# Kernel tuning notes

Measured on AMD Instinct MI355X. Metric: run time of the kernel, lower is better.

## Reference

```python
import jax, jax.numpy as jnp
import numpy as np

N_NODES = 50000
N_EDGES = 800000
K = 8
D_IN = 64
D_OUT = 64


def setup_inputs() -> dict:
    key = jax.random.key(0)
    k1, k2, k3, k4 = jax.random.split(key, 4)
    x = jax.random.normal(k1, (N_NODES, D_IN), dtype=jnp.float32)
    edge_index = jax.random.randint(k2, (2, N_EDGES), 0, N_NODES, dtype=jnp.int64)
    edge_weight = jax.random.uniform(k3, (N_EDGES,), dtype=jnp.float32)
    W = jax.random.normal(k4, (K, D_IN, D_OUT), dtype=jnp.float32) / np.sqrt(D_IN)
    b = jnp.zeros((K, D_OUT), dtype=jnp.float32)
    return {"x": x, "edge_index": edge_index, "edge_weight": edge_weight, "W": W, "b": b}


def reference(x, edge_index, edge_weight, W, b):
    # GCNConv with add_self_loops=True, normalize=True, applied K times in parallel.
    N = x.shape[0]
    loop = jnp.arange(N, dtype=edge_index.dtype)
    src = jnp.concatenate([edge_index[0], loop])           # [E+N] message sources
    dst = jnp.concatenate([edge_index[1], loop])           # [E+N] aggregation targets
    ew = jnp.concatenate([edge_weight, jnp.ones((N,), x.dtype)])  # self-loop weight 1
    # symmetric normalization: deg computed on target index
    deg = jax.ops.segment_sum(ew, dst, num_segments=N)
    dinv = jnp.where(deg > 0, jax.lax.rsqrt(deg), 0.0)
    norm = dinv[src] * ew * dinv[dst]                      # [E+N]
    outs = []
    for k in range(W.shape[0]):                            # fixed small K, structurally distinct params
        h = x @ W[k]                                       # [N, D_OUT]
        agg = jax.ops.segment_sum(norm[:, None] * h[src], dst, num_segments=N)
        outs.append(agg + b[k])
    return jnp.stack(outs, axis=1)                         # [N, K, D_OUT]
```

## Files before the change

kernel.cpp:

```cpp
#include <hip/hip_runtime.h>

#define NN 50000
#define NE 800000

typedef unsigned long long u64;
typedef __attribute__((ext_vector_type(8))) short bf16x8;
typedef __attribute__((ext_vector_type(4))) float f32x4;

#define FXS 33554432.0f
#define FXI (1.0f / 33554432.0f)

__device__ inline unsigned short bf16rne(float f) {
    unsigned u = __float_as_uint(f);
    unsigned r = (u + 0x7FFFu + ((u >> 16) & 1u)) >> 16;
    return (unsigned short)r;
}

__global__ void k_prep(const float* __restrict__ W, u64* __restrict__ hist,
                       ushort* __restrict__ wswz) {
    int t = blockIdx.x * blockDim.x + threadIdx.x;
    if (t < NN) hist[t] = 0ULL;
    if (t < 4096) {
        int l    = t & 63;
        int tile = (t >> 6) & 3;
        int s    = (t >> 8) & 1;
        int h    = t >> 9;
        int c0   = s * 32 + (l >> 4) * 8;
        int col  = tile * 16 + (l & 15);
        unsigned o[8];
#pragma unroll
        for (int r = 0; r < 8; r++)
            o[r] = bf16rne(W[(h * 64 + c0 + r) * 64 + col]);
        uint4 v = make_uint4(o[0] | (o[1] << 16), o[2] | (o[3] << 16),
                             o[4] | (o[5] << 16), o[6] | (o[7] << 16));
        ((uint4*)wswz)[t] = v;
    }
}

__global__ void k_hist(const int* __restrict__ ei, const float* __restrict__ ew,
                       u64* __restrict__ hist, int2* __restrict__ bucket, int E) {
    int t = blockIdx.x * blockDim.x + threadIdx.x;
    int e = t * 2;
    if (e >= E) return;
    int2   s2 = *(const int2*)(ei + e);
    int2   d2 = *(const int2*)(ei + E + e);
    float2 w2 = *(const float2*)(ew + e);
    {
        unsigned fx = (unsigned)(w2.x * FXS + 0.5f);
        u64 old = atomicAdd(&hist[d2.x], ((u64)1 << 40) | (u64)fx);
        unsigned pos = (unsigned)(old >> 40);
        if (pos < 64u) bucket[((unsigned)d2.x << 6) + pos] = make_int2(s2.x, __float_as_int(w2.x));
    }
    {
        unsigned fx = (unsigned)(w2.y * FXS + 0.5f);
        u64 old = atomicAdd(&hist[d2.y], ((u64)1 << 40) | (u64)fx);
        unsigned pos = (unsigned)(old >> 40);
        if (pos < 64u) bucket[((unsigned)d2.y << 6) + pos] = make_int2(s2.y, __float_as_int(w2.y));
    }
}

__global__ void k_dinv(const u64* __restrict__ hist, float* __restrict__ dinv, int n) {
    int i = blockIdx.x * blockDim.x + threadIdx.x;
    if (i < n) {
        u64 h = hist[i];
        dinv[i] = rsqrtf(1.0f + (float)(h & 0xFFFFFFFFFFULL) * FXI);
    }
}

__global__ __launch_bounds__(256) void k_agg(const float* __restrict__ x,
                                             const float* __restrict__ dinv,
                                             const u64* __restrict__ hist,
                                             const int4* __restrict__ bucket4,
                                             ushort* __restrict__ xaggb, int n) {
    int node = blockIdx.x * 4 + (threadIdx.x >> 6);
    if (node >= n) return;
    int lane = threadIdx.x & 63;
    int sub  = lane & 15;
    int grp  = lane >> 4;
    u64 h = hist[node];
    int cnt = (int)(h >> 40);
    if (cnt > 64) cnt = 64;
    float dn = dinv[node];
    f32x4 accA = {0.f, 0.f, 0.f, 0.f};
    f32x4 accB = {0.f, 0.f, 0.f, 0.f};

    const int4* brow = bucket4 + ((size_t)node << 5);
    int4 r0 = brow[0], r1 = brow[1], r2 = brow[2], r3 = brow[3];

    for (int base = 0; base < cnt; base += 8) {
        int4 q0 = r0, q1 = r1, q2 = r2, q3 = r3;
        if (base + 8 < cnt) {
            int nb = (base >> 1) + 4;
            r0 = brow[nb]; r1 = brow[nb + 1]; r2 = brow[nb + 2]; r3 = brow[nb + 3];
        }
        int   s[8]  = { q0.x, q0.z, q1.x, q1.z, q2.x, q2.z, q3.x, q3.z };
        float wv[8] = { __int_as_float(q0.y), __int_as_float(q0.w),
                        __int_as_float(q1.y), __int_as_float(q1.w),
                        __int_as_float(q2.y), __int_as_float(q2.w),
                        __int_as_float(q3.y), __int_as_float(q3.w) };
        bool  vA = (base + grp)     < cnt;
        bool  vB = (base + grp + 4) < cnt;
        int   sA = vA ? s[grp]      : node;
        int   sB = vB ? s[grp + 4]  : node;
        float wA = vA ? wv[grp]     : 0.f;
        float wB = vB ? wv[grp + 4] : 0.f;
        float nA = (dn * dinv[sA]) * wA;
        float nB = (dn * dinv[sB]) * wB;
        f32x4 gA = *(const f32x4*)(x + ((unsigned)sA << 6) + (sub << 2));
        f32x4 gB = *(const f32x4*)(x + ((unsigned)sB << 6) + (sub << 2));
        accA += nA * gA;
        accB += nB * gB;
    }
    f32x4 tt = accA + accB;
#pragma unroll
    for (int m = 16; m <= 32; m <<= 1) {
        tt.x += __shfl_xor(tt.x, m, 64);
        tt.y += __shfl_xor(tt.y, m, 64);
        tt.z += __shfl_xor(tt.z, m, 64);
        tt.w += __shfl_xor(tt.w, m, 64);
    }
    if (grp == 0) {
        f32x4 xs = *(const f32x4*)(x + ((unsigned)node << 6) + (sub << 2));
        f32x4 res = tt + (dn * dn) * xs;
        ushort4 o = make_ushort4(bf16rne(res.x), bf16rne(res.y),
                                 bf16rne(res.z), bf16rne(res.w));
        *(ushort4*)(xaggb + ((unsigned)node << 6) + (sub << 2)) = o;
    }
}

__global__ __launch_bounds__(256) void k_gemm(const ushort* __restrict__ xaggb,
                                              const ushort* __restrict__ wswz,
                                              const float* __restrict__ bb,
                                              float* __restrict__ out, int n) {
    int wave = threadIdx.x >> 6;
    int lane = threadIdx.x & 63;
    int l15  = lane & 15;
    int ksub = lane >> 4;
    int n0   = blockIdx.x * 16;

    bf16x8 a0 = *(const bf16x8*)(xaggb + (size_t)(n0 + l15) * 64 + ksub * 8);
    bf16x8 a1 = *(const bf16x8*)(xaggb + (size_t)(n0 + l15) * 64 + 32 + ksub * 8);

#pragma unroll
    for (int hh = 0; hh < 2; hh++) {
        int h = wave * 2 + hh;
#pragma unroll
        for (int tl = 0; tl < 4; tl++) {
            bf16x8 b0 = *(const bf16x8*)(wswz + (size_t)(((h * 2 + 0) * 4 + tl) * 64 + lane) * 8);
            bf16x8 b1 = *(const bf16x8*)(wswz + (size_t)(((h * 2 + 1) * 4 + tl) * 64 + lane) * 8);
            f32x4 c = {0.f, 0.f, 0.f, 0.f};
            c = __builtin_amdgcn_mfma_f32_16x16x32_bf16(a0, b0, c, 0, 0, 0);
            c = __builtin_amdgcn_mfma_f32_16x16x32_bf16(a1, b1, c, 0, 0, 0);
            int   dout = h * 64 + tl * 16 + l15;
            float bv   = bb[dout];
#pragma unroll
            for (int r = 0; r < 4; r++) {
                int nd = n0 + (ksub << 2) + r;
                __builtin_nontemporal_store(c[r] + bv, out + (size_t)nd * 512 + dout);
            }
        }
    }
}

extern "C" void kernel_launch(void* const* d_in, const int* in_sizes, int n_in,
                              void* d_out, int out_size, void* d_ws, size_t ws_size,
                              hipStream_t stream) {
    const float* x  = (const float*)d_in[0];
    const int*   ei = (const int*)d_in[1];
    const float* ew = (const float*)d_in[2];
    const float* W  = (const float*)d_in[3];
    const float* b  = (const float*)d_in[4];
    float* out = (float*)d_out;

    char* ws = (char*)d_ws;
    size_t off = 0;
    auto carve = [&](size_t bytes) {
        void* p = ws + off;
        off += (bytes + 255) & ~(size_t)255;
        return p;
    };
    u64*    hist   = (u64*)   carve((size_t)NN * 8);
    int2*   bucket = (int2*)  carve((size_t)NN * 64 * 8);
    float*  dinv   = (float*) carve((size_t)NN * 4);
    ushort* xaggb  = (ushort*)carve((size_t)NN * 64 * 2);
    ushort* wswz   = (ushort*)carve((size_t)4096 * 16);
    (void)ws_size; (void)in_sizes; (void)n_in; (void)out_size;

    k_prep<<<(NN + 255) / 256, 256, 0, stream>>>(W, hist, wswz);
    k_hist<<<(NE / 2 + 255) / 256, 256, 0, stream>>>(ei, ew, hist, bucket, NE);
    k_dinv<<<(NN + 255) / 256, 256, 0, stream>>>(hist, dinv, NN);
    k_agg<<<(NN + 3) / 4, 256, 0, stream>>>(x, dinv, hist, (const int4*)bucket, xaggb, NN);
    k_gemm<<<NN / 16, 256, 0, stream>>>(xaggb, wswz, b, out, NN);
}
```

Before: 116.2 us.

## Fuse aggregation into GEMM via LDS and pack bucket records to 32 bits

The aggregation and GEMM kernels are merged into one: each block aggregates 16 nodes (4 per wave) into an LDS tile of bf16 values, then runs the MFMA GEMM straight from LDS. This removes the xaggb global round trip and one launch. Bucket records shrink from 8 to 4 bytes by packing a 16-bit source index with a 16-bit quantized weight, and the histogram kernel now handles 4 edges per thread with nontemporal stores. The packing only works because node ids fit in 16 bits, and 50000 < 65536 holds for this shape. Quantizing edge weights to 16 bits costs precision, and having each wave process its nodes sequentially lowers parallelism in the aggregation phase.

```diff
diff --git a/kernel.cpp b/kernel.cpp
--- a/kernel.cpp
+++ b/kernel.cpp
@@ -9,6 +9,7 @@
 
 #define FXS 33554432.0f
 #define FXI (1.0f / 33554432.0f)
+#define W16I (1.0f / 65536.0f)
 
 __device__ inline unsigned short bf16rne(float f) {
     unsigned u = __float_as_uint(f);
@@ -38,24 +39,30 @@
 }
 
 __global__ void k_hist(const int* __restrict__ ei, const float* __restrict__ ew,
-                       u64* __restrict__ hist, int2* __restrict__ bucket, int E) {
+                       u64* __restrict__ hist, int* __restrict__ bucket, int E) {
     int t = blockIdx.x * blockDim.x + threadIdx.x;
-    int e = t * 2;
+    int e = t * 4;
     if (e >= E) return;
-    int2   s2 = *(const int2*)(ei + e);
-    int2   d2 = *(const int2*)(ei + E + e);
-    float2 w2 = *(const float2*)(ew + e);
-    {
-        unsigned fx = (unsigned)(w2.x * FXS + 0.5f);
-        u64 old = atomicAdd(&hist[d2.x], ((u64)1 << 40) | (u64)fx);
-        unsigned pos = (unsigned)(old >> 40);
-        if (pos < 64u) bucket[((unsigned)d2.x << 6) + pos] = make_int2(s2.x, __float_as_int(w2.x));
+    int4   s4 = *(const int4*)(ei + e);
+    int4   d4 = *(const int4*)(ei + E + e);
+    float4 w4 = *(const float4*)(ew + e);
+    int   ss[4] = { s4.x, s4.y, s4.z, s4.w };
+    int   dd[4] = { d4.x, d4.y, d4.z, d4.w };
+    float ww[4] = { w4.x, w4.y, w4.z, w4.w };
+    u64 old[4];
+#pragma unroll
+    for (int j = 0; j < 4; j++) {
+        unsigned fx = (unsigned)(ww[j] * FXS + 0.5f);
+        old[j] = atomicAdd(&hist[dd[j]], ((u64)1 << 40) | (u64)fx);
     }
-    {
-        unsigned fx = (unsigned)(w2.y * FXS + 0.5f);
-        u64 old = atomicAdd(&hist[d2.y], ((u64)1 << 40) | (u64)fx);
-        unsigned pos = (unsigned)(old >> 40);
-        if (pos < 64u) bucket[((unsigned)d2.y << 6) + pos] = make_int2(s2.y, __float_as_int(w2.y));
+#pragma unroll
+    for (int j = 0; j < 4; j++) {
+        unsigned pos = (unsigned)(old[j] >> 40);
+        unsigned w16 = (unsigned)(ww[j] * 65536.0f + 0.5f);
+        if (w16 > 65535u) w16 = 65535u;
+        if (pos < 64u)
+            __builtin_nontemporal_store((int)((w16 << 16) | (unsigned)ss[j]),
+                                        &bucket[((unsigned)dd[j] << 6) + pos]);
     }
 }
 
@@ -67,79 +74,74 @@
     }
 }
 
-__global__ __launch_bounds__(256) void k_agg(const float* __restrict__ x,
-                                             const float* __restrict__ dinv,
-                                             const u64* __restrict__ hist,
-                                             const int4* __restrict__ bucket4,
-                                             ushort* __restrict__ xaggb, int n) {
-    int node = blockIdx.x * 4 + (threadIdx.x >> 6);
-    if (node >= n) return;
+__global__ __launch_bounds__(256) void k_fused(const float* __restrict__ x,
+                                               const float* __restrict__ dinv,
+                                               const u64* __restrict__ hist,
+                                               const int4* __restrict__ bucket4,
+                                               const ushort* __restrict__ wswz,
+                                               const float* __restrict__ bb,
+                                               float* __restrict__ out) {
+    __shared__ ushort lds[16][72];
+    int wave = threadIdx.x >> 6;
     int lane = threadIdx.x & 63;
     int sub  = lane & 15;
     int grp  = lane >> 4;
-    u64 h = hist[node];
-    int cnt = (int)(h >> 40);
-    if (cnt > 64) cnt = 64;
-    float dn = dinv[node];
-    f32x4 accA = {0.f, 0.f, 0.f, 0.f};
-    f32x4 accB = {0.f, 0.f, 0.f, 0.f};
-
-    const int4* brow = bucket4 + ((size_t)node << 5);
-    int4 r0 = brow[0], r1 = brow[1], r2 = brow[2], r3 = brow[3];
-
-    for (int base = 0; base < cnt; base += 8) {
-        int4 q0 = r0, q1 = r1, q2 = r2, q3 = r3;
-        if (base + 8 < cnt) {
-            int nb = (base >> 1) + 4;
-            r0 = brow[nb]; r1 = brow[nb + 1]; r2 = brow[nb + 2]; r3 = brow[nb + 3];
-        }
-        int   s[8]  = { q0.x, q0.z, q1.x, q1.z, q2.x, q2.z, q3.x, q3.z };
-        float wv[8] = { __int_as_float(q0.y), __int_as_float(q0.w),
-                        __int_as_float(q1.y), __int_as_float(q1.w),
-                        __int_as_float(q2.y), __int_as_float(q2.w),
-                        __int_as_float(q3.y), __int_as_float(q3.w) };
-        bool  vA = (base + grp)     < cnt;
-        bool  vB = (base + grp + 4) < cnt;
-        int   sA = vA ? s[grp]      : node;
-        int   sB = vB ? s[grp + 4]  : node;
-        float wA = vA ? wv[grp]     : 0.f;
-        float wB = vB ? wv[grp + 4] : 0.f;
-        float nA = (dn * dinv[sA]) * wA;
-        float nB = (dn * dinv[sB]) * wB;
-        f32x4 gA = *(const f32x4*)(x + ((unsigned)sA << 6) + (sub << 2));
-        f32x4 gB = *(const f32x4*)(x + ((unsigned)sB << 6) + (sub << 2));
-        accA += nA * gA;
-        accB += nB * gB;
-    }
-    f32x4 tt = accA + accB;
-#pragma unroll
-    for (int m = 16; m <= 32; m <<= 1) {
-        tt.x += __shfl_xor(tt.x, m, 64);
-        tt.y += __shfl_xor(tt.y, m, 64);
-        tt.z += __shfl_xor(tt.z, m, 64);
-        tt.w += __shfl_xor(tt.w, m, 64);
-    }
-    if (grp == 0) {
-        f32x4 xs = *(const f32x4*)(x + ((unsigned)node << 6) + (sub << 2));
-        f32x4 res = tt + (dn * dn) * xs;
-        ushort4 o = make_ushort4(bf16rne(res.x), bf16rne(res.y),
-                                 bf16rne(res.z), bf16rne(res.w));
-        *(ushort4*)(xaggb + ((unsigned)node << 6) + (sub << 2)) = o;
-    }
-}
-
-__global__ __launch_bounds__(256) void k_gemm(const ushort* __restrict__ xaggb,
-                                              const ushort* __restrict__ wswz,
-                                              const float* __restrict__ bb,
-                                              float* __restrict__ out, int n) {
-    int wave = threadIdx.x >> 6;
-    int lane = threadIdx.x & 63;
-    int l15  = lane & 15;
-    int ksub = lane >> 4;
     int n0   = blockIdx.x * 16;
 
-    bf16x8 a0 = *(const bf16x8*)(xaggb + (size_t)(n0 + l15) * 64 + ksub * 8);
-    bf16x8 a1 = *(const bf16x8*)(xaggb + (size_t)(n0 + l15) * 64 + 32 + ksub * 8);
+    for (int nn = 0; nn < 4; nn++) {
+        int row  = wave * 4 + nn;
+        int node = n0 + row;
+        u64 h = hist[node];
+        int cnt = (int)(h >> 40);
+        if (cnt > 64) cnt = 64;
+        float dn = dinv[node];
+        f32x4 accA = {0.f, 0.f, 0.f, 0.f};
+        f32x4 accB = {0.f, 0.f, 0.f, 0.f};
+        const int4* brow = bucket4 + ((size_t)node << 4);
+        int4 r0 = brow[0], r1 = brow[1];
+        for (int base = 0; base < cnt; base += 8) {
+            int4 q0 = r0, q1 = r1;
+            if (base + 8 < cnt) {
+                int nb = (base >> 2) + 2;
+                r0 = brow[nb]; r1 = brow[nb + 1];
+            }
+            int rec[8] = { q0.x, q0.y, q0.z, q0.w, q1.x, q1.y, q1.z, q1.w };
+            bool  vA = (base + grp)     < cnt;
+            bool  vB = (base + grp + 4) < cnt;
+            int   rA = rec[grp], rB = rec[grp + 4];
+            int   sA = vA ? (rA & 0xFFFF) : node;
+            int   sB = vB ? (rB & 0xFFFF) : node;
+            float wA = vA ? (float)((unsigned)rA >> 16) * W16I : 0.f;
+            float wB = vB ? (float)((unsigned)rB >> 16) * W16I : 0.f;
+            float nA = (dn * dinv[sA]) * wA;
+            float nB = (dn * dinv[sB]) * wB;
+            f32x4 gA = *(const f32x4*)(x + ((unsigned)sA << 6) + (sub << 2));
+            f32x4 gB = *(const f32x4*)(x + ((unsigned)sB << 6) + (sub << 2));
+            accA += nA * gA;
+            accB += nB * gB;
+        }
+        f32x4 tt = accA + accB;
+#pragma unroll
+        for (int m = 16; m <= 32; m <<= 1) {
+            tt.x += __shfl_xor(tt.x, m, 64);
+            tt.y += __shfl_xor(tt.y, m, 64);
+            tt.z += __shfl_xor(tt.z, m, 64);
+            tt.w += __shfl_xor(tt.w, m, 64);
+        }
+        if (grp == 0) {
+            f32x4 xs = *(const f32x4*)(x + ((unsigned)node << 6) + (sub << 2));
+            f32x4 res = tt + (dn * dn) * xs;
+            ushort4 o = make_ushort4(bf16rne(res.x), bf16rne(res.y),
+                                     bf16rne(res.z), bf16rne(res.w));
+            *(ushort4*)(&lds[row][sub << 2]) = o;
+        }
+    }
+    __syncthreads();
+
+    int l15  = sub;
+    int ksub = grp;
+    bf16x8 a0 = *(const bf16x8*)(&lds[l15][ksub * 8]);
+    bf16x8 a1 = *(const bf16x8*)(&lds[l15][32 + ksub * 8]);
 
 #pragma unroll
     for (int hh = 0; hh < 2; hh++) {
@@ -180,15 +182,14 @@
         return p;
     };
     u64*    hist   = (u64*)   carve((size_t)NN * 8);
-    int2*   bucket = (int2*)  carve((size_t)NN * 64 * 8);
+    int*    bucket = (int*)   carve((size_t)NN * 64 * 4);
     float*  dinv   = (float*) carve((size_t)NN * 4);
-    ushort* xaggb  = (ushort*)carve((size_t)NN * 64 * 2);
     ushort* wswz   = (ushort*)carve((size_t)4096 * 16);
     (void)ws_size; (void)in_sizes; (void)n_in; (void)out_size;
 
     k_prep<<<(NN + 255) / 256, 256, 0, stream>>>(W, hist, wswz);
-    k_hist<<<(NE / 2 + 255) / 256, 256, 0, stream>>>(ei, ew, hist, bucket, NE);
+    k_hist<<<(NE / 4 + 255) / 256, 256, 0, stream>>>(ei, ew, hist, bucket, NE);
     k_dinv<<<(NN + 255) / 256, 256, 0, stream>>>(hist, dinv, NN);
-    k_agg<<<(NN + 3) / 4, 256, 0, stream>>>(x, dinv, hist, (const int4*)bucket, xaggb, NN);
-    k_gemm<<<NN / 16, 256, 0, stream>>>(xaggb, wswz, b, out, NN);
+    k_fused<<<NN / 16, 256, 0, stream>>>(x, dinv, hist, (const int4*)bucket,
+                                         wswz, b, out);
 }
```

Measured after the change: 138.0 us. 1.19x slower.
